# Kernel optimization log

Hardware: AMD Instinct MI355X
Metric: run time of the kernel (lower is better)

Reference implementation:

```python
import jax, jax.numpy as jnp
import numpy as np

N = 50000   # nodes
E = 400000  # edges (before self-loops)
F = 128     # num_features
H = 8       # heads (layer 1)
C = 64      # hidden_channels
B = 64      # graphs in batch
K = 10      # num_classes
NEG_SLOPE = 0.2


def setup_inputs() -> dict:
    key = jax.random.key(0)
    ks = jax.random.split(key, 12)
    g = lambda k, shape, fan: jax.random.normal(k, shape, jnp.float32) / np.sqrt(fan).astype(np.float32)
    return {
        "x": jax.random.normal(ks[0], (N, F), jnp.float32),
        "edge_index": jax.random.randint(ks[1], (2, E), 0, N, jnp.int32),
        "batch": jnp.sort(jax.random.randint(ks[2], (N,), 0, B, jnp.int32)),
        "W1": g(ks[3], (F, H * C), F),
        "att_src1": g(ks[4], (H, C), C),
        "att_dst1": g(ks[5], (H, C), C),
        "b1": jnp.zeros((H * C,), jnp.float32),
        "W2": g(ks[6], (H * C, C), H * C),
        "att_src2": g(ks[7], (1, C), C),
        "att_dst2": g(ks[8], (1, C), C),
        "b2": jnp.zeros((C,), jnp.float32),
        "lin1_w": g(ks[9], (C, C), C),
        "lin1_b": jnp.zeros((C,), jnp.float32),
        "lin2_w": g(ks[10], (C, K), C),
        "lin2_b": jnp.zeros((K,), jnp.float32),
    }


def gat_conv(x, src, dst, W, att_src, att_dst, bias):
    """PyG GATConv (self-loops already appended to src/dst). x:[N,Fin] -> [N,H*C]."""
    heads, out_c = att_src.shape
    h = (x @ W).reshape(N, heads, out_c)                      # [N,H,C]
    a_s = jnp.einsum('nhc,hc->nh', h, att_src)                # [N,H]
    a_d = jnp.einsum('nhc,hc->nh', h, att_dst)
    e = jax.nn.leaky_relu(a_s[src] + a_d[dst], NEG_SLOPE)     # [E',H]
    # segment softmax over incoming edges of each destination node
    m = jax.ops.segment_max(e, dst, num_segments=N)
    e = jnp.exp(e - m[dst])
    denom = jax.ops.segment_sum(e, dst, num_segments=N)
    alpha = e / (denom[dst] + 1e-16)                          # [E',H]
    out = jax.ops.segment_sum(h[src] * alpha[:, :, None], dst, num_segments=N)  # [N,H,C]
    return out.reshape(N, heads * out_c) + bias


def reference(x, edge_index, batch, W1, att_src1, att_dst1, b1,
              W2, att_src2, att_dst2, b2, lin1_w, lin1_b, lin2_w, lin2_b):
    loops = jnp.arange(N, dtype=edge_index.dtype)
    src = jnp.concatenate([edge_index[0], loops])
    dst = jnp.concatenate([edge_index[1], loops])

    h = gat_conv(x, src, dst, W1, att_src1, att_dst1, b1)     # [N, H*C]
    h = jax.nn.elu(h)                                         # dropout inactive (eval)
    h = gat_conv(h, src, dst, W2, att_src2, att_dst2, b2)     # [N, C]
    h = jax.nn.elu(h)

    pooled = jax.ops.segment_sum(h, batch, num_segments=B)    # global_add_pool -> [B, C]
    z = jax.nn.elu(pooled @ lin1_w + lin1_b)
    logits = z @ lin2_w + lin2_b
    return jax.nn.log_softmax(logits, axis=-1)
```

## Files before the change

### kernel.cpp

```cpp
#include <hip/hip_runtime.h>
#include <hip/hip_bf16.h>

#define DEV static __device__ __forceinline__

constexpr int F1 = 128;
constexpr int H1 = 8;
constexpr int C  = 64;
constexpr int B  = 64;
constexpr int K  = 10;
constexpr float NEG = 0.2f;

typedef __attribute__((ext_vector_type(8))) short short8;
typedef __attribute__((ext_vector_type(4))) float floatx4;

DEV float b2f(__hip_bfloat16 x) { return __bfloat162float(x); }
DEV float elu1(float v) { return v > 0.f ? v : (__expf(v) - 1.f); }
DEV unsigned short f2bbits(float f) {
  __hip_bfloat16 b = __float2bfloat16(f);
  return *(unsigned short*)&b;
}
DEV float blo(unsigned u) { return __uint_as_float(u << 16); }
DEV float bhi(unsigned u) { return __uint_as_float(u & 0xffff0000u); }
DEV float bu(unsigned short u) { return __uint_as_float(((unsigned)u) << 16); }
DEV unsigned pack2(float lo, float hi) {
  return (unsigned)f2bbits(lo) | ((unsigned)f2bbits(hi) << 16);
}


DEV int detect_dev(const void* xraw, int* lds) {
  if (threadIdx.x == 0) {
    const __hip_bfloat16* xb = (const __hip_bfloat16*)xraw;
    int bad = 0;
    for (int i = 0; i < 128; ++i) {
      float v = b2f(xb[2 * i]);
      if (!(fabsf(v) < 1e4f)) bad++;
    }
    *lds = (bad < 13) ? 1 : 0;
  }
  __syncthreads();
  return *lds;
}

#define CVT(p, i) (isbf ? b2f(((const __hip_bfloat16*)(p))[i]) : ((const float*)(p))[i])

__global__ void fused_prep_kernel(const void* x_raw, const void* w1raw,
                                  const void* as1r, const void* ad1r, const void* b1r,
                                  const void* w2raw,
                                  const void* as2r, const void* ad2r, const void* b2r,
                                  const void* l1wr, const void* l1br,
                                  const void* l2wr, const void* l2br,
                                  unsigned short* __restrict__ xbf,
                                  unsigned short* __restrict__ w1frag,
                                  unsigned short* __restrict__ w2frag,
                                  float* __restrict__ wts,
                                  int* __restrict__ deg,
                                  float* __restrict__ pooled,
                                  int nX, int N) {
  __shared__ int fl;
  int isbf = detect_dev(x_raw, &fl);
  int gid = blockIdx.x * 256 + threadIdx.x;
  int stride = gridDim.x * 256;

  if (isbf) {
    const unsigned short* src = (const unsigned short*)x_raw;
    for (int i = gid; i < nX; i += stride) xbf[i] = src[i];
  } else {
    const float* src = (const float*)x_raw;
    for (int i = gid; i < nX; i += stride) xbf[i] = f2bbits(src[i]);
  }
  for (int i = gid; i < 512;  i += stride) wts[0    + i] = CVT(as1r, i);
  for (int i = gid; i < 512;  i += stride) wts[512  + i] = CVT(ad1r, i);
  for (int i = gid; i < 512;  i += stride) {
    int hp = i >> 7, l16 = (i >> 3) & 15, nt = i & 7;
    int c = hp * 128 + nt * 16 + l16;
    wts[1024 + i] = CVT(b1r, c);
  }
  for (int i = gid; i < 64;   i += stride) wts[1536 + i] = CVT(as2r, i);
  for (int i = gid; i < 64;   i += stride) wts[1600 + i] = CVT(ad2r, i);
  for (int i = gid; i < 64;   i += stride) wts[1664 + i] = CVT(b2r, i);
  for (int i = gid; i < 4096; i += stride) wts[1728 + i] = CVT(l1wr, i);
  for (int i = gid; i < 64;   i += stride) wts[5824 + i] = CVT(l1br, i);
  for (int i = gid; i < 640;  i += stride) wts[5888 + i] = CVT(l2wr, i);
  for (int i = gid; i < 10;   i += stride) wts[6528 + i] = CVT(l2br, i);
  for (int t = gid; t < 8192; t += stride) {
    int lane = t & 63, ks = (t >> 6) & 3, nt = t >> 8;
    for (int j = 0; j < 8; ++j) {
      int k = ks * 32 + (lane >> 4) * 8 + j;
      int n = nt * 16 + (lane & 15);
      w1frag[t * 8 + j] = f2bbits(CVT(w1raw, k * 512 + n));
    }
  }
  for (int t = gid; t < 4096; t += stride) {
    int lane = t & 63, nt = (t >> 6) & 3, ks = t >> 8;
    for (int j = 0; j < 8; ++j) {
      int p = ks * 32 + (lane >> 4) * 8 + j;
      int hp = p >> 7, pl16 = (p >> 3) & 15, pnt = p & 7;
      int k = hp * 128 + pnt * 16 + pl16;
      int n = nt * 16 + (lane & 15);
      w2frag[t * 8 + j] = f2bbits(CVT(w2raw, k * 64 + n));
    }
  }
  for (int i = gid; i < N; i += stride) deg[i] = 0;
  for (int i = gid; i < B * C; i += stride) pooled[i] = 0.f;
}

__global__ void deg_count_kernel(const int* __restrict__ ei, int E, int Etot,
                                 int* __restrict__ deg) {
  int e = blockIdx.x * blockDim.x + threadIdx.x;
  if (e >= Etot) return;
  int d = (e < E) ? ei[E + e] : e - E;
  atomicAdd(&deg[d], 1);
}

__global__ void scan_block_kernel(const int* __restrict__ deg,
                                  int* __restrict__ local,
                                  int* __restrict__ bsum, int N) {
  __shared__ int tmp[256];
  int t = threadIdx.x;
  int i = blockIdx.x * 256 + t;
  int v = (i < N) ? deg[i] : 0;
  tmp[t] = v;
  __syncthreads();
  for (int off = 1; off < 256; off <<= 1) {
    int u = (t >= off) ? tmp[t - off] : 0;
    __syncthreads();
    tmp[t] += u;
    __syncthreads();
  }
  if (i < N) local[i] = tmp[t] - v;
  if (t == 255) bsum[blockIdx.x] = tmp[255];
}

__global__ void scan_finish_kernel(const int* __restrict__ local,
                                   const int* __restrict__ bsum, int nb,
                                   int* __restrict__ rowptr,
                                   int* __restrict__ cursor, int N, int Etot) {
  __shared__ int tmp[256];
  __shared__ int offs;
  int t = threadIdx.x;
  int v0 = (t < nb) ? bsum[t] : 0;
  tmp[t] = v0;
  __syncthreads();
  for (int off = 1; off < 256; off <<= 1) {
    int u = (t >= off) ? tmp[t - off] : 0;
    __syncthreads();
    tmp[t] += u;
    __syncthreads();
  }
  if (t == (int)blockIdx.x) offs = tmp[t] - v0;
  __syncthreads();
  int i = blockIdx.x * 256 + t;
  if (i < N) {
    int r = local[i] + offs;
    rowptr[i] = r;
    cursor[i] = r;
  }
  if (i == 0) rowptr[N] = Etot;
}

__global__ __launch_bounds__(256) void gemm1_fill_kernel(
    const unsigned short* __restrict__ xbf,
    const unsigned short* __restrict__ W1frag,
    const float* __restrict__ att_src,
    const float* __restrict__ att_dst,
    unsigned short* __restrict__ h1,
    float* __restrict__ a_s, float* __restrict__ a_d,
    const int* __restrict__ ei, int E, int Etot,
    int* __restrict__ cursor, int* __restrict__ col,
    int gb, int N) {
  __shared__ __align__(16) unsigned short Xls[64 * 136];
  int t = threadIdx.x;

  if ((int)blockIdx.x >= gb) {
    int e = ((int)blockIdx.x - gb) * 256 + t;
    if (e < Etot) {
      int s, d;
      if (e < E) { s = ei[e]; d = ei[E + e]; } else { s = d = e - E; }
      int pos = atomicAdd(&cursor[d], 1);
      col[pos] = s;
    }
    return;
  }

  int w = t >> 6, lane = t & 63;
  int quad = lane >> 4, l16 = lane & 15;
  int blkbase = blockIdx.x * 64;
  int rowbase = blkbase + w * 16;

  for (int idx = t; idx < 1024; idx += 256) {
    int row = idx >> 4, c = idx & 15;
    int rg = blkbase + row; if (rg >= N) rg = N - 1;
    *(uint4*)&Xls[row * 136 + c * 8] =
        *(const uint4*)(xbf + (size_t)rg * 128 + c * 8);
  }
  __syncthreads();

  short8 afr[4];
  {
    int rl = w * 16 + l16;
#pragma unroll
    for (int ks = 0; ks < 4; ++ks)
      afr[ks] = *(const short8*)&Xls[rl * 136 + ks * 32 + quad * 8];
  }

  for (int hp = 0; hp < 4; ++hp) {
    floatx4 acc[8] = {};
    const unsigned short* Bp = W1frag + (size_t)hp * 16384;
#pragma unroll
    for (int nt = 0; nt < 8; ++nt)
#pragma unroll
      for (int ks = 0; ks < 4; ++ks) {
        short8 b = *(const short8*)&Bp[((nt * 4 + ks) * 64 + lane) * 8];
        acc[nt] = __builtin_amdgcn_mfma_f32_16x16x32_bf16(afr[ks], b, acc[nt], 0, 0, 0);
      }

    float asw[8], adw[8];
#pragma unroll
    for (int nt = 0; nt < 8; ++nt) {
      asw[nt] = att_src[hp * 128 + nt * 16 + l16];
      adw[nt] = att_dst[hp * 128 + nt * 16 + l16];
    }
    float ps[2][4] = {}, pd[2][4] = {};
#pragma unroll
    for (int nt = 0; nt < 8; ++nt) {
      int hl = nt >> 2;
#pragma unroll
      for (int r = 0; r < 4; ++r) {
        ps[hl][r] += acc[nt][r] * asw[nt];
        pd[hl][r] += acc[nt][r] * adw[nt];
      }
    }
#pragma unroll
    for (int hl = 0; hl < 2; ++hl)
#pragma unroll
      for (int r = 0; r < 4; ++r) {
        float p = ps[hl][r], q = pd[hl][r];
#pragma unroll
        for (int off = 1; off < 16; off <<= 1) {
          p += __shfl_xor(p, off);
          q += __shfl_xor(q, off);
        }
        int row = rowbase + quad * 4 + r;
        if (l16 == 0 && row < N) {
          a_s[(size_t)row * 8 + hp * 2 + hl] = p;
          a_d[(size_t)row * 8 + hp * 2 + hl] = q;
        }
      }

#pragma unroll
    for (int r = 0; r < 4; ++r) {
      int row = rowbase + quad * 4 + r;
      if (row < N) {
        uint4 o;
        o.x = pack2(acc[0][r], acc[1][r]);
        o.y = pack2(acc[2][r], acc[3][r]);
        o.z = pack2(acc[4][r], acc[5][r]);
        o.w = pack2(acc[6][r], acc[7][r]);
        *(uint4*)&h1[(size_t)row * 512 + hp * 128 + l16 * 8] = o;
      }
    }
  }
}

__global__ __launch_bounds__(256) void gemm2_mfma_kernel(
    const unsigned short* __restrict__ x2bf,
    const unsigned short* __restrict__ W2frag,
    const float* __restrict__ att_src,
    const float* __restrict__ att_dst,
    unsigned short* __restrict__ h2,
    float* __restrict__ a_s, float* __restrict__ a_d,
    int N) {
  int t = threadIdx.x;
  int w = t >> 6, lane = t & 63;
  int quad = lane >> 4, l16 = lane & 15;
  int rowbase = blockIdx.x * 64 + w * 16;

  floatx4 acc[4] = {};
  int r0 = rowbase + l16; if (r0 >= N) r0 = N - 1;
  const unsigned short* p0 = x2bf + (size_t)r0 * 512 + quad * 8;
#pragma unroll
  for (int ks = 0; ks < 16; ++ks) {
    short8 a0 = *(const short8*)(p0 + ks * 32);
#pragma unroll
    for (int nt = 0; nt < 4; ++nt) {
      short8 b = *(const short8*)&W2frag[((ks * 4 + nt) * 64 + lane) * 8];
      acc[nt] = __builtin_amdgcn_mfma_f32_16x16x32_bf16(a0, b, acc[nt], 0, 0, 0);
    }
  }

  float asw[4], adw[4];
#pragma unroll
  for (int nt = 0; nt < 4; ++nt) {
    asw[nt] = att_src[nt * 16 + l16];
    adw[nt] = att_dst[nt * 16 + l16];
  }
  float ps[4] = {}, pd[4] = {};
#pragma unroll
  for (int nt = 0; nt < 4; ++nt)
#pragma unroll
    for (int r = 0; r < 4; ++r) {
      float v = acc[nt][r];
      int row = rowbase + quad * 4 + r;
      if (row < N) h2[(size_t)row * 64 + nt * 16 + l16] = f2bbits(v);
      ps[r] += v * asw[nt];
      pd[r] += v * adw[nt];
    }
#pragma unroll
  for (int r = 0; r < 4; ++r) {
    float p = ps[r], q = pd[r];
#pragma unroll
    for (int off = 1; off < 16; off <<= 1) {
      p += __shfl_xor(p, off);
      q += __shfl_xor(q, off);
    }
    int row = rowbase + quad * 4 + r;
    if (l16 == 0 && row < N) {
      a_s[row] = p;
      a_d[row] = q;
    }
  }
}

__global__ void gat_agg8_kernel(const int* __restrict__ rowptr,
                                const int* __restrict__ col,
                                const float* __restrict__ a_s,
                                const float* __restrict__ a_d,
                                const unsigned short* __restrict__ hfeat,
                                const float* __restrict__ bias,
                                unsigned short* __restrict__ out, int N) {
  int wave = threadIdx.x >> 6, lane = threadIdx.x & 63;
  int d = blockIdx.x * 4 + wave;
  if (d >= N) return;
  int beg = rowptr[d], end = rowptr[d + 1];
  int hh0 = (lane >> 4) * 2, hh1 = hh0 + 1;
  float adh0 = a_d[(size_t)d * 8 + hh0];
  float adh1 = a_d[(size_t)d * 8 + hh1];

  const uint4* hf = (const uint4*)hfeat;
  float acc[8] = {};
  float ws0 = 0.f, ws1 = 0.f;
#pragma unroll 4
  for (int i = beg; i < end; ++i) {
    int s = col[i];
    float e0 = a_s[(size_t)s * 8 + hh0] + adh0;
    e0 = e0 > 0.f ? e0 : NEG * e0;
    float w0 = __expf(e0);
    float e1 = a_s[(size_t)s * 8 + hh1] + adh1;
    e1 = e1 > 0.f ? e1 : NEG * e1;
    float w1 = __expf(e1);
    ws0 += w0; ws1 += w1;
    uint4 q = hf[(size_t)s * 64 + lane];
    acc[0] += w0 * blo(q.x); acc[1] += w0 * bhi(q.x);
    acc[2] += w0 * blo(q.y); acc[3] += w0 * bhi(q.y);
    acc[4] += w1 * blo(q.z); acc[5] += w1 * bhi(q.z);
    acc[6] += w1 * blo(q.w); acc[7] += w1 * bhi(q.w);
  }
  float wi0 = 1.f / (ws0 + 1e-16f), wi1 = 1.f / (ws1 + 1e-16f);
  const float4* b4 = (const float4*)bias;
  float4 b0 = b4[2 * lane], b1 = b4[2 * lane + 1];
  float v0 = elu1(acc[0] * wi0 + b0.x), v1 = elu1(acc[1] * wi0 + b0.y);
  float v2 = elu1(acc[2] * wi0 + b0.z), v3 = elu1(acc[3] * wi0 + b0.w);
  float v4 = elu1(acc[4] * wi1 + b1.x), v5 = elu1(acc[5] * wi1 + b1.y);
  float v6 = elu1(acc[6] * wi1 + b1.z), v7 = elu1(acc[7] * wi1 + b1.w);
  uint4 o;
  o.x = pack2(v0, v1); o.y = pack2(v2, v3);
  o.z = pack2(v4, v5); o.w = pack2(v6, v7);
  ((uint4*)out)[(size_t)d * 64 + lane] = o;
}

__global__ void gat_agg1_kernel(const int* __restrict__ rowptr,
                                const int* __restrict__ col,
                                const float* __restrict__ a_s,
                                const float* __restrict__ a_d,
                                const unsigned short* __restrict__ hfeat,
                                const float* __restrict__ bias,
                                unsigned short* __restrict__ out, int N) {
  int wave = threadIdx.x >> 6, lane = threadIdx.x & 63;
  int d = blockIdx.x * 4 + wave;
  if (d >= N) return;
  int beg = rowptr[d], end = rowptr[d + 1];
  int qg = lane >> 4, l16 = lane & 15;
  float adv = a_d[d];
  const uint2* hfu = (const uint2*)hfeat;
  float acc[4] = {};
  float wsum = 0.f;
#pragma unroll 2
  for (int i = beg + qg; i < end; i += 4) {
    int s = col[i];
    float v = a_s[s] + adv;
    v = v > 0.f ? v : NEG * v;
    float wv = __expf(v);
    wsum += wv;
    uint2 u = hfu[(size_t)s * 16 + l16];
    acc[0] += wv * blo(u.x); acc[1] += wv * bhi(u.x);
    acc[2] += wv * blo(u.y); acc[3] += wv * bhi(u.y);
  }
#pragma unroll
  for (int off = 16; off <= 32; off <<= 1) {
#pragma unroll
    for (int j = 0; j < 4; ++j) acc[j] += __shfl_xor(acc[j], off);
    wsum += __shfl_xor(wsum, off);
  }
  float winv = 1.f / (wsum + 1e-16f);
  float4 bb = ((const float4*)bias)[l16];
  float r0 = elu1(acc[0] * winv + bb.x), r1 = elu1(acc[1] * winv + bb.y);
  float r2 = elu1(acc[2] * winv + bb.z), r3 = elu1(acc[3] * winv + bb.w);
  if (qg == 0) {
    uint2 o; o.x = pack2(r0, r1); o.y = pack2(r2, r3);
    ((uint2*)out)[(size_t)d * 16 + l16] = o;
  }
}

__global__ void pool_kernel(const unsigned short* __restrict__ out2,
                            const int* __restrict__ batch,
                            float* __restrict__ pooled, int N) {
  int wave = threadIdx.x >> 6, lane = threadIdx.x & 63;
  int seg = blockIdx.x * 4 + wave;
  int start = seg * 16;
  if (start >= N) return;
  int end = min(start + 16, N);
  int cur = batch[start];
  float acc = 0.f;
  for (int n = start; n < end; ++n) {
    int bn = batch[n];
    if (bn != cur) {
      unsafeAtomicAdd(&pooled[cur * 64 + lane], acc);
      acc = 0.f; cur = bn;
    }
    acc += bu(out2[(size_t)n * 64 + lane]);
  }
  unsafeAtomicAdd(&pooled[cur * 64 + lane], acc);
}

__global__ void head_kernel(const float* __restrict__ pooled,
                            const float* __restrict__ lin1_w,
                            const float* __restrict__ lin1_b,
                            const float* __restrict__ lin2_w,
                            const float* __restrict__ lin2_b,
                            const void* __restrict__ x_raw,
                            void* __restrict__ outv) {
  __shared__ float P[C];
  __shared__ float Zs[C];
  __shared__ float Ls[K];
  __shared__ float lse_s;
  __shared__ int fl;
  int isbf = detect_dev(x_raw, &fl);
  int g = blockIdx.x, t = threadIdx.x;
  P[t] = pooled[g * C + t];
  __syncthreads();
  float acc = lin1_b[t];
  for (int k = 0; k < C; ++k) acc += P[k] * lin1_w[k * C + t];
  Zs[t] = elu1(acc);
  __syncthreads();
  if (t < K) {
    float a = lin2_b[t];
    for (int k = 0; k < C; ++k) a += Zs[k] * lin2_w[k * K + t];
    Ls[t] = a;
  }
  __syncthreads();
  if (t == 0) {
    float mx = -1e30f;
    for (int c = 0; c < K; ++c) mx = fmaxf(mx, Ls[c]);
    float s = 0.f;
    for (int c = 0; c < K; ++c) s += __expf(Ls[c] - mx);
    lse_s = mx + __logf(s);
  }
  __syncthreads();
  if (t < K) {
    float val = Ls[t] - lse_s;
    if (isbf) ((__hip_bfloat16*)outv)[g * K + t] = __float2bfloat16(val);
    else      ((float*)outv)[g * K + t] = val;
  }
}

extern "C" void kernel_launch(void* const* d_in, const int* in_sizes, int n_in,
                              void* d_out, int out_size, void* d_ws, size_t ws_size,
                              hipStream_t stream) {
  const void* x_raw = d_in[0];
  const int*  ei    = (const int*)d_in[1];
  const int*  batch = (const int*)d_in[2];

  const int N    = in_sizes[2];
  const int E    = in_sizes[1] / 2;
  const int Etot = E + N;
  const int nb   = (N + 255) / 256;

  float* ws   = (float*)d_ws;
  size_t off  = 0;

  float* wts = ws + off; off += 6544;
  float* as1w = wts + 0;
  float* ad1w = wts + 512;
  float* b1w  = wts + 1024;
  float* as2w = wts + 1536;
  float* ad2w = wts + 1600;
  float* b2w  = wts + 1664;
  float* l1w  = wts + 1728;
  float* l1b  = wts + 5824;
  float* l2w  = wts + 5888;
  float* l2b  = wts + 6528;

  unsigned short* xbf    = (unsigned short*)(ws + off); off += (size_t)N * 64;
  unsigned short* w1frag = (unsigned short*)(ws + off); off += 32768;
  unsigned short* w2frag = (unsigned short*)(ws + off); off += 16384;
  unsigned short* h1bf   = (unsigned short*)(ws + off); off += (size_t)N * 256;
  unsigned short* out1bf = (unsigned short*)(ws + off); off += (size_t)N * 256;
  unsigned short* h2bf   = (unsigned short*)(ws + off); off += (size_t)N * 32;
  unsigned short* out2bf = (unsigned short*)(ws + off); off += (size_t)N * 32;
  float* as1  = ws + off; off += (size_t)N * H1;
  float* ad1  = ws + off; off += (size_t)N * H1;
  float* as2  = ws + off; off += (size_t)N;
  float* ad2  = ws + off; off += (size_t)N;
  float* pooled = ws + off; off += (size_t)B * C;

  int* ibase  = (int*)(ws + off);
  int* deg    = ibase;                 ibase += N;
  int* cursor = ibase;                 ibase += N;
  int* rowptr = ibase;                 ibase += N + 1;
  int* locals = ibase;                 ibase += N;
  int* bsum   = ibase;                 ibase += 256;
  int* col    = ibase;                 ibase += Etot;

  fused_prep_kernel<<<1024, 256, 0, stream>>>(
      x_raw, d_in[3], d_in[4], d_in[5], d_in[6], d_in[7], d_in[8], d_in[9],
      d_in[10], d_in[11], d_in[12], d_in[13], d_in[14],
      xbf, w1frag, w2frag, wts, deg, pooled, in_sizes[0], N);

  deg_count_kernel<<<(Etot + 255) / 256, 256, 0, stream>>>(ei, E, Etot, deg);
  scan_block_kernel<<<nb, 256, 0, stream>>>(deg, locals, bsum, N);
  scan_finish_kernel<<<nb, 256, 0, stream>>>(locals, bsum, nb, rowptr, cursor, N, Etot);

  {
    int gb = (N + 63) / 64;
    int fb = (Etot + 255) / 256;
    gemm1_fill_kernel<<<gb + fb, 256, 0, stream>>>(xbf, w1frag, as1w, ad1w,
                                                   h1bf, as1, ad1,
                                                   ei, E, Etot, cursor, col, gb, N);
  }

  gat_agg8_kernel<<<(N + 3) / 4, 256, 0, stream>>>(rowptr, col, as1, ad1, h1bf, b1w, out1bf, N);

  gemm2_mfma_kernel<<<(N + 63) / 64, 256, 0, stream>>>(out1bf, w2frag, as2w, ad2w,
                                                       h2bf, as2, ad2, N);
  gat_agg1_kernel<<<(N + 3) / 4, 256, 0, stream>>>(rowptr, col, as2, ad2, h2bf, b2w, out2bf, N);

  pool_kernel<<<(N + 63) / 64, 256, 0, stream>>>(out2bf, batch, pooled, N);
  head_kernel<<<B, 64, 0, stream>>>(pooled, l1w, l1b, l2w, l2b, x_raw, (void*)d_out);
}
```

Measured before the change: 303.3 us.

## Aggregate raw input features before layer-1 projection to shrink gather traffic

Measured after the change: 332.0 us. +9.5%, slower.

```diff
diff --git a/kernel.cpp b/kernel.cpp
--- a/kernel.cpp
+++ b/kernel.cpp
@@ -158,30 +158,15 @@
   if (i == 0) rowptr[N] = Etot;
 }
 
-__global__ __launch_bounds__(256) void gemm1_fill_kernel(
+__global__ __launch_bounds__(256) void gemm1_att_kernel(
     const unsigned short* __restrict__ xbf,
     const unsigned short* __restrict__ W1frag,
     const float* __restrict__ att_src,
     const float* __restrict__ att_dst,
-    unsigned short* __restrict__ h1,
     float* __restrict__ a_s, float* __restrict__ a_d,
-    const int* __restrict__ ei, int E, int Etot,
-    int* __restrict__ cursor, int* __restrict__ col,
-    int gb, int N) {
+    int N) {
   __shared__ __align__(16) unsigned short Xls[64 * 136];
   int t = threadIdx.x;
-
-  if ((int)blockIdx.x >= gb) {
-    int e = ((int)blockIdx.x - gb) * 256 + t;
-    if (e < Etot) {
-      int s, d;
-      if (e < E) { s = ei[e]; d = ei[E + e]; } else { s = d = e - E; }
-      int pos = atomicAdd(&cursor[d], 1);
-      col[pos] = s;
-    }
-    return;
-  }
-
   int w = t >> 6, lane = t & 63;
   int quad = lane >> 4, l16 = lane & 15;
   int blkbase = blockIdx.x * 64;
@@ -246,18 +231,120 @@
           a_d[(size_t)row * 8 + hp * 2 + hl] = q;
         }
       }
-
-#pragma unroll
-    for (int r = 0; r < 4; ++r) {
-      int row = rowbase + quad * 4 + r;
-      if (row < N) {
-        uint4 o;
-        o.x = pack2(acc[0][r], acc[1][r]);
-        o.y = pack2(acc[2][r], acc[3][r]);
-        o.z = pack2(acc[4][r], acc[5][r]);
-        o.w = pack2(acc[6][r], acc[7][r]);
-        *(uint4*)&h1[(size_t)row * 512 + hp * 128 + l16 * 8] = o;
-      }
+  }
+}
+
+__global__ void fill_weight_kernel(const int* __restrict__ ei, int E, int Etot,
+                                   const float* __restrict__ a_s,
+                                   const float* __restrict__ a_d,
+                                   int* __restrict__ cursor,
+                                   int* __restrict__ col,
+                                   float* __restrict__ wedge) {
+  int e = blockIdx.x * 256 + threadIdx.x;
+  if (e >= Etot) return;
+  int s, d;
+  if (e < E) { s = ei[e]; d = ei[E + e]; } else { s = d = e - E; }
+  int pos = atomicAdd(&cursor[d], 1);
+  col[pos] = s;
+  float4 s0 = *(const float4*)(a_s + (size_t)s * 8);
+  float4 s1 = *(const float4*)(a_s + (size_t)s * 8 + 4);
+  float4 d0 = *(const float4*)(a_d + (size_t)d * 8);
+  float4 d1 = *(const float4*)(a_d + (size_t)d * 8 + 4);
+  float4 w0, w1;
+  float v;
+  v = s0.x + d0.x; v = v > 0.f ? v : NEG * v; w0.x = __expf(v);
+  v = s0.y + d0.y; v = v > 0.f ? v : NEG * v; w0.y = __expf(v);
+  v = s0.z + d0.z; v = v > 0.f ? v : NEG * v; w0.z = __expf(v);
+  v = s0.w + d0.w; v = v > 0.f ? v : NEG * v; w0.w = __expf(v);
+  v = s1.x + d1.x; v = v > 0.f ? v : NEG * v; w1.x = __expf(v);
+  v = s1.y + d1.y; v = v > 0.f ? v : NEG * v; w1.y = __expf(v);
+  v = s1.z + d1.z; v = v > 0.f ? v : NEG * v; w1.z = __expf(v);
+  v = s1.w + d1.w; v = v > 0.f ? v : NEG * v; w1.w = __expf(v);
+  *(float4*)(wedge + (size_t)pos * 8)     = w0;
+  *(float4*)(wedge + (size_t)pos * 8 + 4) = w1;
+}
+
+__global__ __launch_bounds__(256) void aggx_gemm1_kernel(
+    const unsigned short* __restrict__ xbf,
+    const unsigned short* __restrict__ W1frag,
+    const int* __restrict__ rowptr,
+    const int* __restrict__ col,
+    const float* __restrict__ wedge,
+    const float* __restrict__ bias_perm,
+    unsigned short* __restrict__ out1,
+    int N) {
+  __shared__ __align__(16) unsigned short Agg[8 * 16 * 136];
+  int t = threadIdx.x, w = t >> 6, lane = t & 63;
+  int dbase = blockIdx.x * 16;
+  const unsigned* xd = (const unsigned*)xbf;
+  unsigned* AggU = (unsigned*)Agg;
+
+  for (int j = 0; j < 4; ++j) {
+    int dloc = w * 4 + j;
+    int d = dbase + dloc;
+    int dd = d < N ? d : N - 1;
+    int beg = rowptr[dd], end = rowptr[dd + 1];
+    float acc[16] = {};
+    float dn[8] = {};
+#pragma unroll 4
+    for (int i = beg; i < end; ++i) {
+      int iu = __builtin_amdgcn_readfirstlane(i);
+      int s = col[iu];
+      unsigned xv = xd[(size_t)s * 64 + lane];
+      float4 wa = *(const float4*)(wedge + (size_t)iu * 8);
+      float4 wb = *(const float4*)(wedge + (size_t)iu * 8 + 4);
+      float x0 = blo(xv), x1 = bhi(xv);
+      acc[0]  += wa.x * x0; acc[1]  += wa.x * x1; dn[0] += wa.x;
+      acc[2]  += wa.y * x0; acc[3]  += wa.y * x1; dn[1] += wa.y;
+      acc[4]  += wa.z * x0; acc[5]  += wa.z * x1; dn[2] += wa.z;
+      acc[6]  += wa.w * x0; acc[7]  += wa.w * x1; dn[3] += wa.w;
+      acc[8]  += wb.x * x0; acc[9]  += wb.x * x1; dn[4] += wb.x;
+      acc[10] += wb.y * x0; acc[11] += wb.y * x1; dn[5] += wb.y;
+      acc[12] += wb.z * x0; acc[13] += wb.z * x1; dn[6] += wb.z;
+      acc[14] += wb.w * x0; acc[15] += wb.w * x1; dn[7] += wb.w;
+    }
+#pragma unroll
+    for (int h = 0; h < 8; ++h) {
+      float inv = 1.f / (dn[h] + 1e-16f);
+      AggU[(h * 16 + dloc) * 68 + lane] =
+          pack2(acc[2 * h] * inv, acc[2 * h + 1] * inv);
+    }
+  }
+  __syncthreads();
+
+  int quad = lane >> 4, l16 = lane & 15;
+  int hp = w;
+  short8 afr[2][4];
+#pragma unroll
+  for (int hh = 0; hh < 2; ++hh) {
+    int h = hp * 2 + hh;
+#pragma unroll
+    for (int ks = 0; ks < 4; ++ks)
+      afr[hh][ks] = *(const short8*)&Agg[(h * 16 + l16) * 136 + ks * 32 + quad * 8];
+  }
+  floatx4 acc2[8] = {};
+  const unsigned short* Bp = W1frag + (size_t)hp * 16384;
+#pragma unroll
+  for (int nt = 0; nt < 8; ++nt) {
+    int hh = nt >> 2;
+#pragma unroll
+    for (int ks = 0; ks < 4; ++ks) {
+      short8 b = *(const short8*)&Bp[((nt * 4 + ks) * 64 + lane) * 8];
+      acc2[nt] = __builtin_amdgcn_mfma_f32_16x16x32_bf16(afr[hh][ks], b, acc2[nt], 0, 0, 0);
+    }
+  }
+  float4 b0 = *(const float4*)&bias_perm[hp * 128 + l16 * 8];
+  float4 b1 = *(const float4*)&bias_perm[hp * 128 + l16 * 8 + 4];
+#pragma unroll
+  for (int r = 0; r < 4; ++r) {
+    int row = dbase + quad * 4 + r;
+    if (row < N) {
+      uint4 o;
+      o.x = pack2(elu1(acc2[0][r] + b0.x), elu1(acc2[1][r] + b0.y));
+      o.y = pack2(elu1(acc2[2][r] + b0.z), elu1(acc2[3][r] + b0.w));
+      o.z = pack2(elu1(acc2[4][r] + b1.x), elu1(acc2[5][r] + b1.y));
+      o.w = pack2(elu1(acc2[6][r] + b1.z), elu1(acc2[7][r] + b1.w));
+      *(uint4*)&out1[(size_t)row * 512 + hp * 128 + l16 * 8] = o;
     }
   }
 }
@@ -319,53 +406,6 @@
       a_d[row] = q;
     }
   }
-}
-
-__global__ void gat_agg8_kernel(const int* __restrict__ rowptr,
-                                const int* __restrict__ col,
-                                const float* __restrict__ a_s,
-                                const float* __restrict__ a_d,
-                                const unsigned short* __restrict__ hfeat,
-                                const float* __restrict__ bias,
-                                unsigned short* __restrict__ out, int N) {
-  int wave = threadIdx.x >> 6, lane = threadIdx.x & 63;
-  int d = blockIdx.x * 4 + wave;
-  if (d >= N) return;
-  int beg = rowptr[d], end = rowptr[d + 1];
-  int hh0 = (lane >> 4) * 2, hh1 = hh0 + 1;
-  float adh0 = a_d[(size_t)d * 8 + hh0];
-  float adh1 = a_d[(size_t)d * 8 + hh1];
-
-  const uint4* hf = (const uint4*)hfeat;
-  float acc[8] = {};
-  float ws0 = 0.f, ws1 = 0.f;
-#pragma unroll 4
-  for (int i = beg; i < end; ++i) {
-    int s = col[i];
-    float e0 = a_s[(size_t)s * 8 + hh0] + adh0;
-    e0 = e0 > 0.f ? e0 : NEG * e0;
-    float w0 = __expf(e0);
-    float e1 = a_s[(size_t)s * 8 + hh1] + adh1;
-    e1 = e1 > 0.f ? e1 : NEG * e1;
-    float w1 = __expf(e1);
-    ws0 += w0; ws1 += w1;
-    uint4 q = hf[(size_t)s * 64 + lane];
-    acc[0] += w0 * blo(q.x); acc[1] += w0 * bhi(q.x);
-    acc[2] += w0 * blo(q.y); acc[3] += w0 * bhi(q.y);
-    acc[4] += w1 * blo(q.z); acc[5] += w1 * bhi(q.z);
-    acc[6] += w1 * blo(q.w); acc[7] += w1 * bhi(q.w);
-  }
-  float wi0 = 1.f / (ws0 + 1e-16f), wi1 = 1.f / (ws1 + 1e-16f);
-  const float4* b4 = (const float4*)bias;
-  float4 b0 = b4[2 * lane], b1 = b4[2 * lane + 1];
-  float v0 = elu1(acc[0] * wi0 + b0.x), v1 = elu1(acc[1] * wi0 + b0.y);
-  float v2 = elu1(acc[2] * wi0 + b0.z), v3 = elu1(acc[3] * wi0 + b0.w);
-  float v4 = elu1(acc[4] * wi1 + b1.x), v5 = elu1(acc[5] * wi1 + b1.y);
-  float v6 = elu1(acc[6] * wi1 + b1.z), v7 = elu1(acc[7] * wi1 + b1.w);
-  uint4 o;
-  o.x = pack2(v0, v1); o.y = pack2(v2, v3);
-  o.z = pack2(v4, v5); o.w = pack2(v6, v7);
-  ((uint4*)out)[(size_t)d * 64 + lane] = o;
 }
 
 __global__ void gat_agg1_kernel(const int* __restrict__ rowptr,
@@ -503,7 +543,7 @@
   unsigned short* xbf    = (unsigned short*)(ws + off); off += (size_t)N * 64;
   unsigned short* w1frag = (unsigned short*)(ws + off); off += 32768;
   unsigned short* w2frag = (unsigned short*)(ws + off); off += 16384;
-  unsigned short* h1bf   = (unsigned short*)(ws + off); off += (size_t)N * 256;
+  float* wedge           = ws + off;                    off += (size_t)Etot * 8;
   unsigned short* out1bf = (unsigned short*)(ws + off); off += (size_t)N * 256;
   unsigned short* h2bf   = (unsigned short*)(ws + off); off += (size_t)N * 32;
   unsigned short* out2bf = (unsigned short*)(ws + off); off += (size_t)N * 32;
@@ -530,15 +570,14 @@
   scan_block_kernel<<<nb, 256, 0, stream>>>(deg, locals, bsum, N);
   scan_finish_kernel<<<nb, 256, 0, stream>>>(locals, bsum, nb, rowptr, cursor, N, Etot);
 
-  {
-    int gb = (N + 63) / 64;
-    int fb = (Etot + 255) / 256;
-    gemm1_fill_kernel<<<gb + fb, 256, 0, stream>>>(xbf, w1frag, as1w, ad1w,
-                                                   h1bf, as1, ad1,
-                                                   ei, E, Etot, cursor, col, gb, N);
-  }
-
-  gat_agg8_kernel<<<(N + 3) / 4, 256, 0, stream>>>(rowptr, col, as1, ad1, h1bf, b1w, out1bf, N);
+  gemm1_att_kernel<<<(N + 63) / 64, 256, 0, stream>>>(xbf, w1frag, as1w, ad1w,
+                                                      as1, ad1, N);
+
+  fill_weight_kernel<<<(Etot + 255) / 256, 256, 0, stream>>>(
+      ei, E, Etot, as1, ad1, cursor, col, wedge);
+
+  aggx_gemm1_kernel<<<(N + 15) / 16, 256, 0, stream>>>(
+      xbf, w1frag, rowptr, col, wedge, b1w, out1bf, N);
 
   gemm2_mfma_kernel<<<(N + 63) / 64, 256, 0, stream>>>(out1bf, w2frag, as2w, ad2w,
                                                        h2bf, as2, ad2, N);
```
